# Performance work log

Measured on AMD Instinct MI355X. Metric: run time of the kernel, lower is better.

## Reference

```python
import jax, jax.numpy as jnp
import numpy as np

B, H, S, D = 2, 16, 2048, 64


def setup_inputs() -> dict:
    key = jax.random.key(0)
    kq, kk, kv = jax.random.split(key, 3)
    query = jax.random.normal(kq, (B, H, S, D), dtype=jnp.float32)
    k_ = jax.random.normal(kk, (B, H, S, D), dtype=jnp.float32)
    value = jax.random.normal(kv, (B, H, S, D), dtype=jnp.float32)
    # causal mask, broadcastable to (B, H, S, S); 0 => masked out
    mask = jnp.tril(jnp.ones((S, S), dtype=jnp.int32))[None, None, :, :]
    return {"query": query, "key": k_, "value": value, "mask": mask}


def reference(query, key, value, mask):
    dim = key.shape[-1]
    # scores: [b, h, s_q, s_k]
    scores = jnp.einsum('bhqe,bhke->bhqk', query, key) * (dim ** -0.5)
    scores = jnp.where(mask == 0, -jnp.inf, scores)
    attention = jax.nn.softmax(scores, axis=-1)
    output = jnp.einsum('bhqk,bhkd->bhqd', attention, value)
    return output, attention
```

## Files before the change

kernel.cpp:

```cpp
#include <hip/hip_runtime.h>

#define S_LEN 2048
#define DHEAD 64
#define NQT   32
#define SCALE_LOG2E 0.18033688011112042f

typedef __bf16 bf16_t;
typedef bf16_t bf16x8 __attribute__((ext_vector_type(8)));
typedef bf16_t bf16x4 __attribute__((ext_vector_type(4)));
typedef float  f32x4  __attribute__((ext_vector_type(4)));

static __device__ __forceinline__ f32x4 mfma16(bf16x8 a, bf16x8 b, f32x4 c) {
    return __builtin_amdgcn_mfma_f32_16x16x32_bf16(a, b, c, 0, 0, 0);
}

static __device__ __forceinline__ int sw(int row, int colByte) {
    return (row << 7) + (colByte ^ ((row & 7) << 4));
}

template <bool SCALE>
static __device__ __forceinline__ void stage_tile(const float* __restrict__ src,
                                                  char* dst, int tid) {
#pragma unroll
    for (int i = 0; i < 2; ++i) {
        int f = tid + (i << 8);
        int r = f >> 3;
        int c = (f & 7) << 3;
        const f32x4* sp = (const f32x4*)(src + r * 64 + c);
        f32x4 a = sp[0], b = sp[1];
        if (SCALE) { a = a * SCALE_LOG2E; b = b * SCALE_LOG2E; }
        bf16x8 v;
        v[0] = (bf16_t)a[0]; v[1] = (bf16_t)a[1]; v[2] = (bf16_t)a[2]; v[3] = (bf16_t)a[3];
        v[4] = (bf16_t)b[0]; v[5] = (bf16_t)b[1]; v[6] = (bf16_t)b[2]; v[7] = (bf16_t)b[3];
        *(bf16x8*)(dst + sw(r, c << 1)) = v;
    }
}

static __device__ __forceinline__ void stage_vt(const float* __restrict__ src,
                                                char* dst, int tid) {
    int k0 = (tid >> 4) << 2;
    int d0 = (tid & 15) << 2;
    f32x4 r0 = *(const f32x4*)(src + (k0 + 0) * 64 + d0);
    f32x4 r1 = *(const f32x4*)(src + (k0 + 1) * 64 + d0);
    f32x4 r2 = *(const f32x4*)(src + (k0 + 2) * 64 + d0);
    f32x4 r3 = *(const f32x4*)(src + (k0 + 3) * 64 + d0);
#pragma unroll
    for (int j = 0; j < 4; ++j) {
        int d = d0 + j;
        bf16x4 w;
        w[0] = (bf16_t)r0[j]; w[1] = (bf16_t)r1[j];
        w[2] = (bf16_t)r2[j]; w[3] = (bf16_t)r3[j];
        *(bf16x4*)(dst + (d << 7) + ((k0 << 1) ^ ((d & 7) << 4))) = w;
    }
}

extern "C" __global__ void __launch_bounds__(256)
attn_fused(const float* __restrict__ Q, const float* __restrict__ K,
           const float* __restrict__ V, float* __restrict__ out,
           float* __restrict__ att) {
    __shared__ __align__(16) char QsB[8192];
    __shared__ __align__(16) char KsB[8192];
    __shared__ __align__(16) char VtB[8192];
    __shared__ __align__(16) char PsB[4][2048];

    const int tid  = threadIdx.x;
    const int bid  = blockIdx.x;
    const int bh   = bid & 31;
    const int qt   = 31 - (bid >> 5);
    const int lane = tid & 63;
    const int wq   = tid >> 6;
    const int g    = lane >> 4;
    const int qc   = lane & 15;

    const size_t hoff = (size_t)bh * (S_LEN * DHEAD);
    const float* Qb = Q + hoff;
    const float* Kb = K + hoff;
    const float* Vb = V + hoff;
    float* outb = out + hoff;
    float* attb = att + (size_t)bh * ((size_t)S_LEN * S_LEN);

    const int q0 = qt << 6;

    {
        f32x4 z = {0.f, 0.f, 0.f, 0.f};
        for (int zt = qt + 1; zt < NQT; ++zt) {
            float* base = attb + (size_t)q0 * S_LEN + (zt << 6);
#pragma unroll
            for (int i = 0; i < 4; ++i) {
                int f = tid + (i << 8);
                int r = f >> 4;
                int c = (f & 15) << 2;
                __builtin_nontemporal_store(z, (f32x4*)(base + (size_t)r * S_LEN + c));
            }
        }
    }

    stage_tile<true>(Qb + q0 * DHEAD, QsB, tid);
    __syncthreads();

    const int qrow = (wq << 4) + qc;
    const int qg   = q0 + qrow;
    bf16x8 bq0 = *(const bf16x8*)(QsB + sw(qrow, (g << 4)));
    bf16x8 bq1 = *(const bf16x8*)(QsB + sw(qrow, 64 + (g << 4)));

    const int nkt = qt + 1;
    float m = -1e30f, l = 0.f;

    for (int kt = 0; kt < nkt; ++kt) {
        __syncthreads();
        stage_tile<false>(Kb + kt * 4096, KsB, tid);
        __syncthreads();
        float sv[16];
#pragma unroll
        for (int kb = 0; kb < 4; ++kb) {
            const int ar = (kb << 4) + qc;
            bf16x8 a0 = *(const bf16x8*)(KsB + sw(ar, (g << 4)));
            bf16x8 a1 = *(const bf16x8*)(KsB + sw(ar, 64 + (g << 4)));
            f32x4 acc = {0.f, 0.f, 0.f, 0.f};
            acc = mfma16(a0, bq0, acc);
            acc = mfma16(a1, bq1, acc);
#pragma unroll
            for (int r = 0; r < 4; ++r) sv[(kb << 2) + r] = acc[r];
        }
        if (kt == qt) {
#pragma unroll
            for (int kb = 0; kb < 4; ++kb)
#pragma unroll
                for (int r = 0; r < 4; ++r) {
                    int kg = (kt << 6) + (kb << 4) + (g << 2) + r;
                    if (kg > qg) sv[(kb << 2) + r] = -1e30f;
                }
        }
        float mx = sv[0];
#pragma unroll
        for (int i = 1; i < 16; ++i) mx = fmaxf(mx, sv[i]);
        mx = fmaxf(mx, __shfl_xor(mx, 16));
        mx = fmaxf(mx, __shfl_xor(mx, 32));
        float mn = fmaxf(m, mx);
        float corr = exp2f(m - mn);
        float se = 0.f;
#pragma unroll
        for (int i = 0; i < 16; ++i) se += exp2f(sv[i] - mn);
        se += __shfl_xor(se, 16);
        se += __shfl_xor(se, 32);
        l = l * corr + se;
        m = mn;
    }

    const float il = 1.0f / l;
    f32x4 oacc[4];
#pragma unroll
    for (int i = 0; i < 4; ++i) oacc[i] = (f32x4){0.f, 0.f, 0.f, 0.f};

    char* PsW = PsB[wq];

    for (int kt = 0; kt < nkt; ++kt) {
        __syncthreads();
        stage_tile<false>(Kb + kt * 4096, KsB, tid);
        stage_vt(Vb + kt * 4096, VtB, tid);
        __syncthreads();
#pragma unroll
        for (int kb = 0; kb < 4; ++kb) {
            const int ar = (kb << 4) + qc;
            bf16x8 a0 = *(const bf16x8*)(KsB + sw(ar, (g << 4)));
            bf16x8 a1 = *(const bf16x8*)(KsB + sw(ar, 64 + (g << 4)));
            f32x4 acc = {0.f, 0.f, 0.f, 0.f};
            acc = mfma16(a0, bq0, acc);
            acc = mfma16(a1, bq1, acc);
            float p[4];
#pragma unroll
            for (int r = 0; r < 4; ++r) {
                float s = acc[r];
                if (kt == qt) {
                    int kg = (kt << 6) + (kb << 4) + (g << 2) + r;
                    if (kg > qg) s = -1e30f;
                }
                p[r] = exp2f(s - m) * il;
            }
            f32x4 pw = {p[0], p[1], p[2], p[3]};
            __builtin_nontemporal_store(
                pw, (f32x4*)(attb + (size_t)qg * S_LEN + (kt << 6) + (kb << 4) + (g << 2)));
            bf16x4 pb;
            pb[0] = (bf16_t)p[0]; pb[1] = (bf16_t)p[1];
            pb[2] = (bf16_t)p[2]; pb[3] = (bf16_t)p[3];
            *(bf16x4*)(PsW + (qc << 7) + (((kb << 5) + (g << 3)) ^ ((qc & 7) << 4))) = pb;
        }
        bf16x8 bp0 = *(const bf16x8*)(PsW + sw(qc, (g << 4)));
        bf16x8 bp1 = *(const bf16x8*)(PsW + sw(qc, 64 + (g << 4)));
#pragma unroll
        for (int dc = 0; dc < 4; ++dc) {
            const int vr = (dc << 4) + qc;
            bf16x8 av0 = *(const bf16x8*)(VtB + sw(vr, (g << 4)));
            bf16x8 av1 = *(const bf16x8*)(VtB + sw(vr, 64 + (g << 4)));
            oacc[dc] = mfma16(av0, bp0, oacc[dc]);
            oacc[dc] = mfma16(av1, bp1, oacc[dc]);
        }
    }

#pragma unroll
    for (int dc = 0; dc < 4; ++dc) {
        f32x4 o = {oacc[dc][0], oacc[dc][1], oacc[dc][2], oacc[dc][3]};
        *(f32x4*)(outb + (size_t)qg * DHEAD + (dc << 4) + (g << 2)) = o;
    }
}

extern "C" void kernel_launch(void* const* d_in, const int* in_sizes, int n_in,
                              void* d_out, int out_size, void* d_ws, size_t ws_size,
                              hipStream_t stream) {
    const float* Q = (const float*)d_in[0];
    const float* K = (const float*)d_in[1];
    const float* V = (const float*)d_in[2];
    float* out = (float*)d_out;
    float* att = out + (size_t)2 * 16 * S_LEN * DHEAD;
    dim3 grid(2 * 16 * NQT);
    dim3 block(256);
    hipLaunchKernelGGL(attn_fused, grid, block, 0, stream, Q, K, V, out, att);
}
```

Measured before the change: 707.7 us.

## Split attention into flash pass and separate tile-parallel probability-writing kernel

The single fused kernel, which ran two serial passes over K per query tile and wrote the attention matrix from a load-imbalanced grid, is replaced by two kernels. The first is a one-pass online-softmax flash kernel that rescales the output accumulator and saves the per-row max and inverse sum to workspace. The second launches one block per (head, q-tile, k-tile), recomputes QK^T for its tile and writes the normalized probabilities, or zeros above the diagonal. This spreads the dominant 512MB attention write over many more blocks at the cost of a second launch, extra Q/K reloads and reliance on workspace.

```diff
diff --git a/kernel.cpp b/kernel.cpp
--- a/kernel.cpp
+++ b/kernel.cpp
@@ -3,6 +3,7 @@
 #define S_LEN 2048
 #define DHEAD 64
 #define NQT   32
+#define BH    32
 #define SCALE_LOG2E 0.18033688011112042f
 
 typedef __bf16 bf16_t;
@@ -55,9 +56,9 @@
 }
 
 extern "C" __global__ void __launch_bounds__(256)
-attn_fused(const float* __restrict__ Q, const float* __restrict__ K,
+attn_flash(const float* __restrict__ Q, const float* __restrict__ K,
            const float* __restrict__ V, float* __restrict__ out,
-           float* __restrict__ att) {
+           float* __restrict__ mrow, float* __restrict__ ilrow) {
     __shared__ __align__(16) char QsB[8192];
     __shared__ __align__(16) char KsB[8192];
     __shared__ __align__(16) char VtB[8192];
@@ -77,23 +78,8 @@
     const float* Kb = K + hoff;
     const float* Vb = V + hoff;
     float* outb = out + hoff;
-    float* attb = att + (size_t)bh * ((size_t)S_LEN * S_LEN);
 
     const int q0 = qt << 6;
-
-    {
-        f32x4 z = {0.f, 0.f, 0.f, 0.f};
-        for (int zt = qt + 1; zt < NQT; ++zt) {
-            float* base = attb + (size_t)q0 * S_LEN + (zt << 6);
-#pragma unroll
-            for (int i = 0; i < 4; ++i) {
-                int f = tid + (i << 8);
-                int r = f >> 4;
-                int c = (f & 15) << 2;
-                __builtin_nontemporal_store(z, (f32x4*)(base + (size_t)r * S_LEN + c));
-            }
-        }
-    }
 
     stage_tile<true>(Qb + q0 * DHEAD, QsB, tid);
     __syncthreads();
@@ -103,13 +89,19 @@
     bf16x8 bq0 = *(const bf16x8*)(QsB + sw(qrow, (g << 4)));
     bf16x8 bq1 = *(const bf16x8*)(QsB + sw(qrow, 64 + (g << 4)));
 
-    const int nkt = qt + 1;
     float m = -1e30f, l = 0.f;
-
-    for (int kt = 0; kt < nkt; ++kt) {
+    f32x4 oacc[4];
+#pragma unroll
+    for (int i = 0; i < 4; ++i) oacc[i] = (f32x4){0.f, 0.f, 0.f, 0.f};
+
+    char* PsW = PsB[wq];
+
+    for (int kt = 0; kt <= qt; ++kt) {
         __syncthreads();
         stage_tile<false>(Kb + kt * 4096, KsB, tid);
+        stage_vt(Vb + kt * 4096, VtB, tid);
         __syncthreads();
+
         float sv[16];
 #pragma unroll
         for (int kb = 0; kb < 4; ++kb) {
@@ -136,53 +128,24 @@
         for (int i = 1; i < 16; ++i) mx = fmaxf(mx, sv[i]);
         mx = fmaxf(mx, __shfl_xor(mx, 16));
         mx = fmaxf(mx, __shfl_xor(mx, 32));
-        float mn = fmaxf(m, mx);
-        float corr = exp2f(m - mn);
-        float se = 0.f;
-#pragma unroll
-        for (int i = 0; i < 16; ++i) se += exp2f(sv[i] - mn);
+        const float mn   = fmaxf(m, mx);
+        const float corr = exp2f(m - mn);
+
+        float p[16], se = 0.f;
+#pragma unroll
+        for (int i = 0; i < 16; ++i) { p[i] = exp2f(sv[i] - mn); se += p[i]; }
         se += __shfl_xor(se, 16);
         se += __shfl_xor(se, 32);
         l = l * corr + se;
         m = mn;
-    }
-
-    const float il = 1.0f / l;
-    f32x4 oacc[4];
-#pragma unroll
-    for (int i = 0; i < 4; ++i) oacc[i] = (f32x4){0.f, 0.f, 0.f, 0.f};
-
-    char* PsW = PsB[wq];
-
-    for (int kt = 0; kt < nkt; ++kt) {
-        __syncthreads();
-        stage_tile<false>(Kb + kt * 4096, KsB, tid);
-        stage_vt(Vb + kt * 4096, VtB, tid);
-        __syncthreads();
+#pragma unroll
+        for (int i = 0; i < 4; ++i) oacc[i] = oacc[i] * corr;
+
 #pragma unroll
         for (int kb = 0; kb < 4; ++kb) {
-            const int ar = (kb << 4) + qc;
-            bf16x8 a0 = *(const bf16x8*)(KsB + sw(ar, (g << 4)));
-            bf16x8 a1 = *(const bf16x8*)(KsB + sw(ar, 64 + (g << 4)));
-            f32x4 acc = {0.f, 0.f, 0.f, 0.f};
-            acc = mfma16(a0, bq0, acc);
-            acc = mfma16(a1, bq1, acc);
-            float p[4];
-#pragma unroll
-            for (int r = 0; r < 4; ++r) {
-                float s = acc[r];
-                if (kt == qt) {
-                    int kg = (kt << 6) + (kb << 4) + (g << 2) + r;
-                    if (kg > qg) s = -1e30f;
-                }
-                p[r] = exp2f(s - m) * il;
-            }
-            f32x4 pw = {p[0], p[1], p[2], p[3]};
-            __builtin_nontemporal_store(
-                pw, (f32x4*)(attb + (size_t)qg * S_LEN + (kt << 6) + (kb << 4) + (g << 2)));
             bf16x4 pb;
-            pb[0] = (bf16_t)p[0]; pb[1] = (bf16_t)p[1];
-            pb[2] = (bf16_t)p[2]; pb[3] = (bf16_t)p[3];
+            pb[0] = (bf16_t)p[(kb << 2) + 0]; pb[1] = (bf16_t)p[(kb << 2) + 1];
+            pb[2] = (bf16_t)p[(kb << 2) + 2]; pb[3] = (bf16_t)p[(kb << 2) + 3];
             *(bf16x4*)(PsW + (qc << 7) + (((kb << 5) + (g << 3)) ^ ((qc & 7) << 4))) = pb;
         }
         bf16x8 bp0 = *(const bf16x8*)(PsW + sw(qc, (g << 4)));
@@ -197,10 +160,82 @@
         }
     }
 
+    const float il = 1.0f / l;
 #pragma unroll
     for (int dc = 0; dc < 4; ++dc) {
-        f32x4 o = {oacc[dc][0], oacc[dc][1], oacc[dc][2], oacc[dc][3]};
+        f32x4 o = oacc[dc] * il;
         *(f32x4*)(outb + (size_t)qg * DHEAD + (dc << 4) + (g << 2)) = o;
+    }
+    if (g == 0) {
+        mrow [bh * S_LEN + qg] = m;
+        ilrow[bh * S_LEN + qg] = il;
+    }
+}
+
+extern "C" __global__ void __launch_bounds__(256)
+attn_probs(const float* __restrict__ Q, const float* __restrict__ K,
+           const float* __restrict__ mrow, const float* __restrict__ ilrow,
+           float* __restrict__ att) {
+    const int tid = threadIdx.x;
+    const int bid = blockIdx.x;
+    const int bh  = bid >> 10;
+    const int qt  = (bid >> 5) & 31;
+    const int kt  = bid & 31;
+
+    float* attb = att + (size_t)bh * ((size_t)S_LEN * S_LEN);
+    const int q0 = qt << 6;
+    const int k0 = kt << 6;
+
+    if (kt > qt) {
+        f32x4 z = {0.f, 0.f, 0.f, 0.f};
+#pragma unroll
+        for (int i = 0; i < 4; ++i) {
+            int f = tid + (i << 8);
+            int r = f >> 4;
+            int c = (f & 15) << 2;
+            __builtin_nontemporal_store(z, (f32x4*)(attb + (size_t)(q0 + r) * S_LEN + k0 + c));
+        }
+        return;
+    }
+
+    __shared__ __align__(16) char QsB[8192];
+    __shared__ __align__(16) char KsB[8192];
+
+    const size_t hoff = (size_t)bh * (S_LEN * DHEAD);
+    stage_tile<true >(Q + hoff + q0 * DHEAD, QsB, tid);
+    stage_tile<false>(K + hoff + k0 * DHEAD, KsB, tid);
+    __syncthreads();
+
+    const int lane = tid & 63;
+    const int wq   = tid >> 6;
+    const int g    = lane >> 4;
+    const int qc   = lane & 15;
+    const int qrow = (wq << 4) + qc;
+    const int qg   = q0 + qrow;
+
+    bf16x8 bq0 = *(const bf16x8*)(QsB + sw(qrow, (g << 4)));
+    bf16x8 bq1 = *(const bf16x8*)(QsB + sw(qrow, 64 + (g << 4)));
+
+    const float m  = mrow [bh * S_LEN + qg];
+    const float il = ilrow[bh * S_LEN + qg];
+
+#pragma unroll
+    for (int kb = 0; kb < 4; ++kb) {
+        const int ar = (kb << 4) + qc;
+        bf16x8 a0 = *(const bf16x8*)(KsB + sw(ar, (g << 4)));
+        bf16x8 a1 = *(const bf16x8*)(KsB + sw(ar, 64 + (g << 4)));
+        f32x4 acc = {0.f, 0.f, 0.f, 0.f};
+        acc = mfma16(a0, bq0, acc);
+        acc = mfma16(a1, bq1, acc);
+        f32x4 pw;
+#pragma unroll
+        for (int r = 0; r < 4; ++r) {
+            int kg = k0 + (kb << 4) + (g << 2) + r;
+            float p = exp2f(acc[r] - m) * il;
+            pw[r] = (kt == qt && kg > qg) ? 0.f : p;
+        }
+        __builtin_nontemporal_store(
+            pw, (f32x4*)(attb + (size_t)qg * S_LEN + k0 + (kb << 4) + (g << 2)));
     }
 }
 
@@ -211,8 +246,12 @@
     const float* K = (const float*)d_in[1];
     const float* V = (const float*)d_in[2];
     float* out = (float*)d_out;
-    float* att = out + (size_t)2 * 16 * S_LEN * DHEAD;
-    dim3 grid(2 * 16 * NQT);
-    dim3 block(256);
-    hipLaunchKernelGGL(attn_fused, grid, block, 0, stream, Q, K, V, out, att);
-}
+    float* att = out + (size_t)BH * S_LEN * DHEAD;
+    float* mrow  = (float*)d_ws;
+    float* ilrow = mrow + (size_t)BH * S_LEN;
+
+    hipLaunchKernelGGL(attn_flash, dim3(BH * NQT), dim3(256), 0, stream,
+                       Q, K, V, out, mrow, ilrow);
+    hipLaunchKernelGGL(attn_probs, dim3(BH * NQT * NQT), dim3(256), 0, stream,
+                       Q, K, mrow, ilrow, att);
+}
```

New measurement: 677.7 us. 4.2% less time.
